# Performance work log

Measured on AMD Instinct MI355X. Metric: run time of the kernel, lower is better.

Reference implementation:

```python
import jax, jax.numpy as jnp
import numpy as np

B, S, D, H = 2, 2048, 2048, 16
Dh = D // H


def _rotate_interleaved(t):
    # t: (..., Dh); pairs (x0,x1) -> (-x1, x0), interleaved
    t2 = t.reshape(t.shape[:-1] + (Dh // 2, 2))
    rot = jnp.stack([-t2[..., 1], t2[..., 0]], axis=-1)
    return rot.reshape(t.shape)


def _apply_rope(t, cos, sin):
    # t: (B,H,S,Dh); cos/sin: (S,Dh) broadcast over batch and heads
    return t * cos[None, None, :, :] + _rotate_interleaved(t) * sin[None, None, :, :]


def setup_inputs() -> dict:
    key = jax.random.key(0)
    ks = jax.random.split(key, 4)
    x = jax.random.normal(ks[0], (B, S, D), dtype=jnp.float32)
    wq = jax.random.normal(ks[1], (D, D), dtype=jnp.float32) * (D ** -0.5)
    wk = jax.random.normal(ks[2], (D, D), dtype=jnp.float32) * (D ** -0.5)
    wv = jax.random.normal(ks[3], (D, D), dtype=jnp.float32) * (D ** -0.5)
    # Real RoPE cos/sin tables: theta_i = 10000^{-2i/Dh}, interleaved layout
    inv_freq = 1.0 / (10000.0 ** (np.arange(0, Dh, 2, dtype=np.float32) / Dh))
    angles = np.arange(S, dtype=np.float32)[:, None] * inv_freq[None, :]  # (S, Dh/2)
    angles = np.repeat(angles, 2, axis=-1)  # (S, Dh) interleaved
    rope_cos = jnp.asarray(np.cos(angles))
    rope_sin = jnp.asarray(np.sin(angles))
    return {"x": x, "wq": wq, "wk": wk, "wv": wv,
            "rope_cos": rope_cos, "rope_sin": rope_sin}


def reference(x, wq, wk, wv, rope_cos, rope_sin):
    b, s, d = x.shape
    # QKV projections (torch Linear: y = x @ W^T), split into heads -> (B,H,S,Dh)
    def proj(w):
        return (x @ w.T).reshape(b, s, H, Dh).transpose(0, 2, 1, 3)
    q, k, v = proj(wq), proj(wk), proj(wv)
    cos, sin = rope_cos[:s], rope_sin[:s]
    q = _apply_rope(q, cos, sin)
    k = _apply_rope(k, cos, sin)
    # causal SDPA
    scores = jnp.einsum('bhqd,bhkd->bhqk', q, k) / jnp.sqrt(jnp.float32(Dh))
    causal = jnp.tril(jnp.ones((s, s), dtype=bool))
    scores = jnp.where(causal[None, None], scores, jnp.float32(-1e30))
    attn = jax.nn.softmax(scores, axis=-1)
    out = jnp.einsum('bhqk,bhkd->bhqd', attn, v)  # (B,H,S,Dh)
    # extra trailing softmax over head dim (as in source)
    out = jax.nn.softmax(out.astype(jnp.float32), axis=-1)
    return out.transpose(0, 2, 1, 3).reshape(b, s, -1)
```

## Files before the change

### kernel.cpp

```cpp
#include <hip/hip_runtime.h>

#define Bc 2
#define Sc 2048
#define Dc 2048
#define Hc 16
#define DHc 128

typedef _Float16 f16;
typedef __attribute__((ext_vector_type(4))) _Float16 v4h;
typedef __attribute__((ext_vector_type(8))) _Float16 v8h;
typedef __attribute__((ext_vector_type(4))) float v4f;
typedef __attribute__((ext_vector_type(16))) float v16f;
typedef __attribute__((ext_vector_type(4))) float f32x4;

__global__ void cvt_kernel(const float* __restrict__ x, const float* __restrict__ wq,
                           const float* __restrict__ wk, const float* __restrict__ wv,
                           f16* __restrict__ xh, f16* __restrict__ wqh,
                           f16* __restrict__ wkh, f16* __restrict__ wvh)
{
    int bid = blockIdx.x;
    const float* src; f16* dst; int idx;
    if (bid < 8192)       { src = x;  dst = xh;  idx = bid; }
    else if (bid < 12288) { src = wq; dst = wqh; idx = bid - 8192; }
    else if (bid < 16384) { src = wk; dst = wkh; idx = bid - 12288; }
    else                  { src = wv; dst = wvh; idx = bid - 16384; }
    int i = idx * 256 + threadIdx.x;
    f32x4 v = ((const f32x4*)src)[i];
    v4h hv; hv[0]=(f16)v[0]; hv[1]=(f16)v[1]; hv[2]=(f16)v[2]; hv[3]=(f16)v[3];
    ((v4h*)dst)[i] = hv;
}

__launch_bounds__(256)
__global__ void proj_f16_kernel(const f16* __restrict__ xh, const f16* __restrict__ wqh,
                                const f16* __restrict__ wkh, const f16* __restrict__ wvh,
                                const float* __restrict__ cs, const float* __restrict__ sn,
                                f16* __restrict__ qh, f16* __restrict__ kh,
                                f16* __restrict__ vt)
{
    const int z = blockIdx.z;
    const f16* wh = (z == 0) ? wqh : ((z == 1) ? wkh : wvh);
    const int m0 = blockIdx.x * 128, n0 = blockIdx.y * 128;
    const int tid = threadIdx.x, lane = tid & 63, wid = tid >> 6;
    const int wm = wid >> 1, wn = wid & 1;
    const int l15 = lane & 15, quad = lane >> 4;
    const int lrow = lane >> 3, lcol = lane & 7;

    __shared__ __align__(16) f16 smem[128 * 136];
    f16 (*As)[64] = (f16(*)[64])smem;
    f16 (*Bs)[64] = (f16(*)[64])(smem + 8192);

    v4f acc[4][4];
    #pragma unroll
    for (int i = 0; i < 4; ++i)
        #pragma unroll
        for (int j = 0; j < 4; ++j)
            acc[i][j] = (v4f){0.f, 0.f, 0.f, 0.f};

    for (int k0 = 0; k0 < Dc; k0 += 64) {
        __syncthreads();
        #pragma unroll
        for (int i = 0; i < 4; ++i) {
            int g = wid * 4 + i;
            const f16* ga = xh + (size_t)(m0 + g * 8 + lrow) * Dc + k0 + lcol * 8;
            __builtin_amdgcn_global_load_lds(
                (const __attribute__((address_space(1))) void*)ga,
                (__attribute__((address_space(3))) void*)(smem + g * 512), 16, 0, 0);
            const f16* gb = wh + (size_t)(n0 + g * 8 + lrow) * Dc + k0 + lcol * 8;
            __builtin_amdgcn_global_load_lds(
                (const __attribute__((address_space(1))) void*)gb,
                (__attribute__((address_space(3))) void*)(smem + 8192 + g * 512), 16, 0, 0);
        }
        __syncthreads();
        #pragma unroll
        for (int kk = 0; kk < 2; ++kk) {
            v8h af[4], bf[4];
            #pragma unroll
            for (int mi = 0; mi < 4; ++mi)
                af[mi] = *(const v8h*)&As[wm * 64 + mi * 16 + l15][kk * 32 + quad * 8];
            #pragma unroll
            for (int ni = 0; ni < 4; ++ni)
                bf[ni] = *(const v8h*)&Bs[wn * 64 + ni * 16 + l15][kk * 32 + quad * 8];
            #pragma unroll
            for (int mi = 0; mi < 4; ++mi)
                #pragma unroll
                for (int ni = 0; ni < 4; ++ni)
                    acc[mi][ni] = __builtin_amdgcn_mfma_f32_16x16x32_f16(
                        af[mi], bf[ni], acc[mi][ni], 0, 0, 0);
        }
    }
    __syncthreads();

    f16 (*Ep)[136] = (f16(*)[136])smem;
    #pragma unroll
    for (int mi = 0; mi < 4; ++mi)
        #pragma unroll
        for (int ni = 0; ni < 4; ++ni)
            #pragma unroll
            for (int r = 0; r < 4; ++r) {
                int ml = wm * 64 + mi * 16 + quad * 4 + r;
                int nl = wn * 64 + ni * 16 + l15;
                f16 val = (f16)acc[mi][ni][r];
                if (z == 2) Ep[nl][ml] = val;
                else        Ep[ml][nl] = val;
            }
    __syncthreads();

    const int b = m0 >> 11, s0 = m0 & 2047, h = n0 >> 7;
    if (z < 2) {
        f16* outp = (z == 0) ? qh : kh;
        const float scl = (z == 0) ? 0.08838834764831845f : 1.0f;
        #pragma unroll
        for (int it = 0; it < 8; ++it) {
            int ch = tid + it * 256, row = ch >> 4, c = ch & 15;
            v8h val = *(const v8h*)&Ep[row][c * 8];
            int s = s0 + row;
            const float* cp = cs + (size_t)s * DHc + c * 8;
            const float* sp = sn + (size_t)s * DHc + c * 8;
            f32x4 ca = *(const f32x4*)cp, cb = *(const f32x4*)(cp + 4);
            f32x4 sa = *(const f32x4*)sp, sb = *(const f32x4*)(sp + 4);
            float v[8];
            #pragma unroll
            for (int j = 0; j < 8; ++j) v[j] = (float)val[j];
            v8h rv;
            rv[0] = (f16)((v[0]*ca[0] - v[1]*sa[0]) * scl);
            rv[1] = (f16)((v[1]*ca[1] + v[0]*sa[1]) * scl);
            rv[2] = (f16)((v[2]*ca[2] - v[3]*sa[2]) * scl);
            rv[3] = (f16)((v[3]*ca[3] + v[2]*sa[3]) * scl);
            rv[4] = (f16)((v[4]*cb[0] - v[5]*sb[0]) * scl);
            rv[5] = (f16)((v[5]*cb[1] + v[4]*sb[1]) * scl);
            rv[6] = (f16)((v[6]*cb[2] - v[7]*sb[2]) * scl);
            rv[7] = (f16)((v[7]*cb[3] + v[6]*sb[3]) * scl);
            *(v8h*)(outp + ((size_t)((b * Hc + h) * Sc) + s0 + row) * DHc + c * 8) = rv;
        }
    } else {
        #pragma unroll
        for (int it = 0; it < 8; ++it) {
            int ch = tid + it * 256, row = ch >> 4, c = ch & 15;
            *(v8h*)(vt + ((size_t)((b * Hc + h) * DHc) + row) * Sc + s0 + c * 8) =
                *(const v8h*)&Ep[row][c * 8];
        }
    }
}

__launch_bounds__(256)
__global__ void proj_kernel(const float* __restrict__ x, const float* __restrict__ wq,
                            const float* __restrict__ wk, const float* __restrict__ wv,
                            f16* __restrict__ qh, f16* __restrict__ kh, f16* __restrict__ vt)
{
    const int z = blockIdx.z;
    const float* w = (z == 0) ? wq : ((z == 1) ? wk : wv);
    const int m0 = blockIdx.x * 128, n0 = blockIdx.y * 128;
    const int tid = threadIdx.x, lane = tid & 63, wid = tid >> 6;
    const int wm = wid >> 1, wn = wid & 1;
    const int l15 = lane & 15, quad = lane >> 4;

    __shared__ __align__(16) f16 smem[2 * 128 * 72];
    f16 (*As)[72] = (f16(*)[72])smem;
    f16 (*Bs)[72] = (f16(*)[72])(smem + 128 * 72);

    v4f acc[4][4];
    for (int i = 0; i < 4; ++i)
        for (int j = 0; j < 4; ++j)
            acc[i][j] = (v4f){0.f, 0.f, 0.f, 0.f};

    for (int k0 = 0; k0 < Dc; k0 += 64) {
        __syncthreads();
        for (int it = 0; it < 4; ++it) {
            int chunk = tid + it * 256;
            int r = chunk >> 3, cc = chunk & 7;
            const f32x4* pa = (const f32x4*)(x + (size_t)(m0 + r) * Dc + k0 + cc * 8);
            f32x4 a0 = pa[0], a1 = pa[1];
            v8h ha;
            ha[0]=(f16)a0[0]; ha[1]=(f16)a0[1]; ha[2]=(f16)a0[2]; ha[3]=(f16)a0[3];
            ha[4]=(f16)a1[0]; ha[5]=(f16)a1[1]; ha[6]=(f16)a1[2]; ha[7]=(f16)a1[3];
            *(v8h*)&As[r][cc * 8] = ha;
            const f32x4* pb = (const f32x4*)(w + (size_t)(n0 + r) * Dc + k0 + cc * 8);
            f32x4 b0 = pb[0], b1 = pb[1];
            v8h hb;
            hb[0]=(f16)b0[0]; hb[1]=(f16)b0[1]; hb[2]=(f16)b0[2]; hb[3]=(f16)b0[3];
            hb[4]=(f16)b1[0]; hb[5]=(f16)b1[1]; hb[6]=(f16)b1[2]; hb[7]=(f16)b1[3];
            *(v8h*)&Bs[r][cc * 8] = hb;
        }
        __syncthreads();
        for (int kk = 0; kk < 2; ++kk) {
            v8h af[4], bf[4];
            for (int mi = 0; mi < 4; ++mi)
                af[mi] = *(const v8h*)&As[wm * 64 + mi * 16 + l15][kk * 32 + quad * 8];
            for (int ni = 0; ni < 4; ++ni)
                bf[ni] = *(const v8h*)&Bs[wn * 64 + ni * 16 + l15][kk * 32 + quad * 8];
            for (int mi = 0; mi < 4; ++mi)
                for (int ni = 0; ni < 4; ++ni)
                    acc[mi][ni] = __builtin_amdgcn_mfma_f32_16x16x32_f16(
                        af[mi], bf[ni], acc[mi][ni], 0, 0, 0);
        }
    }
    __syncthreads();
    f16 (*Ep)[136] = (f16(*)[136])smem;
    for (int mi = 0; mi < 4; ++mi)
        for (int ni = 0; ni < 4; ++ni)
            for (int r = 0; r < 4; ++r) {
                int ml = wm * 64 + mi * 16 + quad * 4 + r;
                int nl = wn * 64 + ni * 16 + l15;
                f16 val = (f16)acc[mi][ni][r];
                if (z == 2) Ep[nl][ml] = val;
                else        Ep[ml][nl] = val;
            }
    __syncthreads();
    const int b = m0 >> 11, s0 = m0 & 2047, h = n0 >> 7;
    if (z < 2) {
        f16* outp = (z == 0) ? qh : kh;
        for (int it = 0; it < 8; ++it) {
            int ch = tid + it * 256, row = ch >> 4, c = ch & 15;
            *(v8h*)(outp + ((size_t)((b * Hc + h) * Sc) + s0 + row) * DHc + c * 8) =
                *(const v8h*)&Ep[row][c * 8];
        }
    } else {
        for (int it = 0; it < 8; ++it) {
            int ch = tid + it * 256, row = ch >> 4, c = ch & 15;
            *(v8h*)(vt + ((size_t)((b * Hc + h) * DHc) + row) * Sc + s0 + c * 8) =
                *(const v8h*)&Ep[row][c * 8];
        }
    }
}

__global__ void rope_kernel(f16* __restrict__ qh, f16* __restrict__ kh,
                            const float* __restrict__ cs, const float* __restrict__ sn)
{
    int i  = blockIdx.x * 256 + threadIdx.x;
    int d2 = i & 63;
    int s  = (i >> 6) & (Sc - 1);
    int bh = i >> 17;
    f16* t = blockIdx.y ? kh : qh;
    float scale = blockIdx.y ? 1.0f : 0.08838834764831845f;
    float c  = cs[s * DHc + 2 * d2];
    float sv = sn[s * DHc + 2 * d2];
    f16* p = t + ((size_t)bh * Sc + s) * DHc + 2 * d2;
    float t0 = (float)p[0], t1 = (float)p[1];
    p[0] = (f16)((t0 * c - t1 * sv) * scale);
    p[1] = (f16)((t1 * c + t0 * sv) * scale);
}

__launch_bounds__(256, 2)
__global__ void attn_kernel(const f16* __restrict__ qh, const f16* __restrict__ kh,
                            const f16* __restrict__ vt, float* __restrict__ out)
{
    const int qt = 15 - blockIdx.x;
    const int bh = blockIdx.y;
    const int b = bh >> 4, h = bh & 15;
    const int tid = threadIdx.x, lane = tid & 63, w = tid >> 6;
    const int l31 = lane & 31, half = lane >> 5;

    __shared__ __align__(16) f16 smem[33792];
    f16* ksm = smem;
    f16* vsm = smem + 16384;

    const int q0 = qt * 128 + w * 32;
    const int qg = q0 + l31;
    const size_t bhoff = (size_t)bh * Sc * DHc;

    v8h qf[8];
    const f16* qrow = qh + bhoff + (size_t)qg * DHc;
    #pragma unroll
    for (int s = 0; s < 8; ++s)
        qf[s] = *(const v8h*)(qrow + s * 16 + half * 8);

    const f16* ksrc[4]; const f16* vsrc[4];
    f16* kdst[4]; f16* vdst[4];
    #pragma unroll
    for (int j = 0; j < 4; ++j) {
        int slot0 = j * 256 + w * 64;
        {   int r = (slot0 >> 4) + (lane >> 4);
            int c = (lane & 15) ^ (r & 7);
            ksrc[j] = kh + bhoff + (size_t)r * DHc + c * 8;
            kdst[j] = ksm + slot0 * 8; }
        {   int r = (slot0 >> 3) + (lane >> 3);
            int c = (lane & 7) ^ (r & 7);
            vsrc[j] = vt + bhoff + (size_t)r * Sc + c * 8;
            vdst[j] = vsm + slot0 * 8; }
    }

#define STAGE(kt_, buf_) do {                                                   \
        int _ko = (kt_) * 64 * DHc;                                             \
        int _vo = (kt_) * 64;                                                   \
        int _lb = (buf_) * 8192;                                                \
        _Pragma("unroll")                                                       \
        for (int j = 0; j < 4; ++j) {                                           \
            __builtin_amdgcn_global_load_lds(                                   \
                (const __attribute__((address_space(1))) void*)(ksrc[j] + _ko), \
                (__attribute__((address_space(3))) void*)(kdst[j] + _lb), 16, 0, 0); \
            __builtin_amdgcn_global_load_lds(                                   \
                (const __attribute__((address_space(1))) void*)(vsrc[j] + _vo), \
                (__attribute__((address_space(3))) void*)(vdst[j] + _lb), 16, 0, 0); \
        } } while (0)

    float l_run = 0.f;
    v16f o[4];
    #pragma unroll
    for (int i = 0; i < 4; ++i)
        #pragma unroll
        for (int r = 0; r < 16; ++r) o[i][r] = 0.f;

    const int sw = l31 & 7;
    const int nkt = 2 * qt + 2;

    STAGE(0, 0);
    for (int kt = 0; kt < nkt; ++kt) {
        __syncthreads();
        const int buf = kt & 1;
        if (kt + 1 < nkt) STAGE(kt + 1, buf ^ 1);
        if (q0 + 31 < kt * 64) continue;

        const f16* kbuf = ksm + buf * 8192;
        const f16* vbuf = vsm + buf * 8192;
        const bool do1 = (kt * 64 + 32 <= q0 + 31);

        v16f st0, st1;
        #pragma unroll
        for (int r = 0; r < 16; ++r) { st0[r] = 0.f; st1[r] = 0.f; }
        #pragma unroll
        for (int s = 0; s < 8; ++s) {
            int c = ((s * 2 + half) ^ sw) * 8;
            v8h kf0 = *(const v8h*)(kbuf + l31 * 128 + c);
            st0 = __builtin_amdgcn_mfma_f32_32x32x16_f16(kf0, qf[s], st0, 0, 0, 0);
            if (do1) {
                v8h kf1 = *(const v8h*)(kbuf + (32 + l31) * 128 + c);
                st1 = __builtin_amdgcn_mfma_f32_32x32x16_f16(kf1, qf[s], st1, 0, 0, 0);
            }
        }

        float sum = 0.f;
        #pragma unroll
        for (int r = 0; r < 16; ++r) {
            int key = kt * 64 + (r & 3) + 8 * (r >> 2) + 4 * half;
            float sv = (key > qg) ? -1e30f : st0[r];
            float p = __expf(sv);
            st0[r] = p; sum += p;
        }
        if (do1) {
            #pragma unroll
            for (int r = 0; r < 16; ++r) {
                int key = kt * 64 + 32 + (r & 3) + 8 * (r >> 2) + 4 * half;
                float sv = (key > qg) ? -1e30f : st1[r];
                float p = __expf(sv);
                st1[r] = p; sum += p;
            }
        }
        sum += __shfl_xor(sum, 32);
        l_run += sum;

        #pragma unroll
        for (int s2 = 0; s2 < 4; ++s2) {
            v4h bfr;
            bfr[0]=(f16)st0[4*s2]; bfr[1]=(f16)st0[4*s2+1];
            bfr[2]=(f16)st0[4*s2+2]; bfr[3]=(f16)st0[4*s2+3];
            int c = ((s2 ^ sw) * 8) + half * 4;
            #pragma unroll
            for (int dt = 0; dt < 4; ++dt) {
                v4h vf = *(const v4h*)(vbuf + (dt * 32 + l31) * 64 + c);
                o[dt] = __builtin_amdgcn_mfma_f32_32x32x8f16(vf, bfr, o[dt], 0, 0, 0);
            }
        }
        if (do1) {
            #pragma unroll
            for (int s2 = 0; s2 < 4; ++s2) {
                v4h bfr;
                bfr[0]=(f16)st1[4*s2]; bfr[1]=(f16)st1[4*s2+1];
                bfr[2]=(f16)st1[4*s2+2]; bfr[3]=(f16)st1[4*s2+3];
                int c = (((4 + s2) ^ sw) * 8) + half * 4;
                #pragma unroll
                for (int dt = 0; dt < 4; ++dt) {
                    v4h vf = *(const v4h*)(vbuf + (dt * 32 + l31) * 64 + c);
                    o[dt] = __builtin_amdgcn_mfma_f32_32x32x8f16(vf, bfr, o[dt], 0, 0, 0);
                }
            }
        }
    }
#undef STAGE

    float inv = 1.f / l_run;
    float mxd = -1e30f;
    #pragma unroll
    for (int dt = 0; dt < 4; ++dt)
        #pragma unroll
        for (int r = 0; r < 16; ++r) {
            o[dt][r] *= inv;
            mxd = fmaxf(mxd, o[dt][r]);
        }
    mxd = fmaxf(mxd, __shfl_xor(mxd, 32));
    float sd = 0.f;
    #pragma unroll
    for (int dt = 0; dt < 4; ++dt)
        #pragma unroll
        for (int r = 0; r < 16; ++r) {
            float t = __expf(o[dt][r] - mxd);
            o[dt][r] = t;
            sd += t;
        }
    sd += __shfl_xor(sd, 32);
    float rinv = 1.f / sd;

    __syncthreads();
    float* os = (float*)smem + w * (32 * 132);
    #pragma unroll
    for (int dt = 0; dt < 4; ++dt)
        #pragma unroll
        for (int r = 0; r < 16; ++r) {
            int dh = dt * 32 + (r & 3) + 8 * (r >> 2) + 4 * half;
            os[l31 * 132 + dh] = o[dt][r] * rinv;
        }
    __syncthreads();
    #pragma unroll
    for (int step = 0; step < 16; ++step) {
        int row = step * 2 + half;
        f32x4 vv = *(const f32x4*)(os - (size_t)half * 0 + row * 132 + l31 * 4);
        *(f32x4*)(out + ((size_t)(b * Sc + q0 + row)) * Dc + h * DHc + l31 * 4) = vv;
    }
}

extern "C" void kernel_launch(void* const* d_in, const int* in_sizes, int n_in,
                              void* d_out, int out_size, void* d_ws, size_t ws_size,
                              hipStream_t stream)
{
    const float* x  = (const float*)d_in[0];
    const float* wq = (const float*)d_in[1];
    const float* wk = (const float*)d_in[2];
    const float* wv = (const float*)d_in[3];
    const float* cs = (const float*)d_in[4];
    const float* sn = (const float*)d_in[5];
    float* out = (float*)d_out;

    const size_t tsz = (size_t)Bc * Hc * Sc * DHc;
    f16* qh = (f16*)d_ws;
    f16* kh = qh + tsz;
    f16* vt = kh + tsz;

    if (ws_size >= 11 * tsz) {
        f16* xh  = vt + tsz;
        f16* wqh = xh + tsz;
        f16* wkh = wqh + tsz / 2;
        f16* wvh = wkh + tsz / 2;
        cvt_kernel<<<20480, 256, 0, stream>>>(x, wq, wk, wv, xh, wqh, wkh, wvh);
        proj_f16_kernel<<<dim3(32, 16, 3), 256, 0, stream>>>(xh, wqh, wkh, wvh,
                                                             cs, sn, qh, kh, vt);
    } else {
        proj_kernel<<<dim3(32, 16, 3), 256, 0, stream>>>(x, wq, wk, wv, qh, kh, vt);
        rope_kernel<<<dim3(16384, 2), 256, 0, stream>>>(qh, kh, cs, sn);
    }
    attn_kernel<<<dim3(16, 32), 256, 0, stream>>>(qh, kh, vt, out);
}
```

Measured before the change: 364.7 us.

## Load K directly from global, shrink LDS to V only, raise occupancy

K fragments are now read straight from global memory per wave instead of being staged through LDS, so shared memory holds only the double-buffered V tiles (32KB instead of ~66KB). The launch bound goes from 2 to 3 blocks per SM. The output epilogue writes float4s from registers to global directly, dropping the LDS transpose and its two barriers. The trade-off is more global/L2 traffic for K, with K loads sitting on the MFMA critical path without prefetch, tighter register limits at 3 blocks, and less coalesced output stores.

```diff
diff --git a/kernel.cpp b/kernel.cpp
--- a/kernel.cpp
+++ b/kernel.cpp
@@ -240,7 +240,7 @@
     p[1] = (f16)((t1 * c + t0 * sv) * scale);
 }
 
-__launch_bounds__(256, 2)
+__launch_bounds__(256, 3)
 __global__ void attn_kernel(const f16* __restrict__ qh, const f16* __restrict__ kh,
                             const f16* __restrict__ vt, float* __restrict__ out)
 {
@@ -250,9 +250,7 @@
     const int tid = threadIdx.x, lane = tid & 63, w = tid >> 6;
     const int l31 = lane & 31, half = lane >> 5;
 
-    __shared__ __align__(16) f16 smem[33792];
-    f16* ksm = smem;
-    f16* vsm = smem + 16384;
+    __shared__ __align__(16) f16 vsm[2 * 8192];
 
     const int q0 = qt * 128 + w * 32;
     const int qg = q0 + l31;
@@ -264,33 +262,22 @@
     for (int s = 0; s < 8; ++s)
         qf[s] = *(const v8h*)(qrow + s * 16 + half * 8);
 
-    const f16* ksrc[4]; const f16* vsrc[4];
-    f16* kdst[4]; f16* vdst[4];
-    #pragma unroll
-    for (int j = 0; j < 4; ++j) {
-        int slot0 = j * 256 + w * 64;
-        {   int r = (slot0 >> 4) + (lane >> 4);
-            int c = (lane & 15) ^ (r & 7);
-            ksrc[j] = kh + bhoff + (size_t)r * DHc + c * 8;
-            kdst[j] = ksm + slot0 * 8; }
-        {   int r = (slot0 >> 3) + (lane >> 3);
-            int c = (lane & 7) ^ (r & 7);
-            vsrc[j] = vt + bhoff + (size_t)r * Sc + c * 8;
-            vdst[j] = vsm + slot0 * 8; }
-    }
-
-#define STAGE(kt_, buf_) do {                                                   \
-        int _ko = (kt_) * 64 * DHc;                                             \
-        int _vo = (kt_) * 64;                                                   \
-        int _lb = (buf_) * 8192;                                                \
-        _Pragma("unroll")                                                       \
-        for (int j = 0; j < 4; ++j) {                                           \
-            __builtin_amdgcn_global_load_lds(                                   \
-                (const __attribute__((address_space(1))) void*)(ksrc[j] + _ko), \
-                (__attribute__((address_space(3))) void*)(kdst[j] + _lb), 16, 0, 0); \
-            __builtin_amdgcn_global_load_lds(                                   \
-                (const __attribute__((address_space(1))) void*)(vsrc[j] + _vo), \
-                (__attribute__((address_space(3))) void*)(vdst[j] + _lb), 16, 0, 0); \
+    const f16* kb0 = kh + bhoff + (size_t)l31 * DHc + half * 8;
+    const f16* kb1 = kb0 + 32 * DHc;
+
+    const int vr = w * 8 + (lane >> 3);
+    const int vc = (lane & 7) ^ ((lane >> 3) & 7);
+    const f16* vsrc0 = vt + bhoff + (size_t)vr * Sc + vc * 8;
+    const int vdst0 = (w * 64) * 8;
+
+#define STAGEV(kt_, buf_) do {                                                     \
+        _Pragma("unroll")                                                          \
+        for (int j = 0; j < 4; ++j) {                                              \
+            __builtin_amdgcn_global_load_lds(                                      \
+                (const __attribute__((address_space(1))) void*)                    \
+                    (vsrc0 + (size_t)(j * 32) * Sc + (kt_) * 64),                  \
+                (__attribute__((address_space(3))) void*)                          \
+                    (vsm + (buf_) * 8192 + vdst0 + j * 2048), 16, 0, 0);           \
         } } while (0)
 
     float l_run = 0.f;
@@ -303,27 +290,27 @@
     const int sw = l31 & 7;
     const int nkt = 2 * qt + 2;
 
-    STAGE(0, 0);
+    STAGEV(0, 0);
     for (int kt = 0; kt < nkt; ++kt) {
         __syncthreads();
         const int buf = kt & 1;
-        if (kt + 1 < nkt) STAGE(kt + 1, buf ^ 1);
+        if (kt + 1 < nkt) STAGEV(kt + 1, buf ^ 1);
         if (q0 + 31 < kt * 64) continue;
 
-        const f16* kbuf = ksm + buf * 8192;
         const f16* vbuf = vsm + buf * 8192;
         const bool do1 = (kt * 64 + 32 <= q0 + 31);
+        const f16* k0p = kb0 + (size_t)kt * 64 * DHc;
+        const f16* k1p = kb1 + (size_t)kt * 64 * DHc;
 
         v16f st0, st1;
         #pragma unroll
         for (int r = 0; r < 16; ++r) { st0[r] = 0.f; st1[r] = 0.f; }
         #pragma unroll
         for (int s = 0; s < 8; ++s) {
-            int c = ((s * 2 + half) ^ sw) * 8;
-            v8h kf0 = *(const v8h*)(kbuf + l31 * 128 + c);
+            v8h kf0 = *(const v8h*)(k0p + s * 16);
             st0 = __builtin_amdgcn_mfma_f32_32x32x16_f16(kf0, qf[s], st0, 0, 0, 0);
             if (do1) {
-                v8h kf1 = *(const v8h*)(kbuf + (32 + l31) * 128 + c);
+                v8h kf1 = *(const v8h*)(k1p + s * 16);
                 st1 = __builtin_amdgcn_mfma_f32_32x32x16_f16(kf1, qf[s], st1, 0, 0, 0);
             }
         }
@@ -375,7 +362,7 @@
             }
         }
     }
-#undef STAGE
+#undef STAGEV
 
     float inv = 1.f / l_run;
     float mxd = -1e30f;
@@ -399,22 +386,18 @@
     sd += __shfl_xor(sd, 32);
     float rinv = 1.f / sd;
 
-    __syncthreads();
-    float* os = (float*)smem + w * (32 * 132);
+    float* orow = out + (size_t)(b * Sc + qg) * Dc + h * DHc;
     #pragma unroll
     for (int dt = 0; dt < 4; ++dt)
         #pragma unroll
-        for (int r = 0; r < 16; ++r) {
-            int dh = dt * 32 + (r & 3) + 8 * (r >> 2) + 4 * half;
-            os[l31 * 132 + dh] = o[dt][r] * rinv;
-        }
-    __syncthreads();
-    #pragma unroll
-    for (int step = 0; step < 16; ++step) {
-        int row = step * 2 + half;
-        f32x4 vv = *(const f32x4*)(os - (size_t)half * 0 + row * 132 + l31 * 4);
-        *(f32x4*)(out + ((size_t)(b * Sc + q0 + row)) * Dc + h * DHc + l31 * 4) = vv;
-    }
+        for (int g = 0; g < 4; ++g) {
+            f32x4 vv;
+            vv[0] = o[dt][4*g+0] * rinv;
+            vv[1] = o[dt][4*g+1] * rinv;
+            vv[2] = o[dt][4*g+2] * rinv;
+            vv[3] = o[dt][4*g+3] * rinv;
+            *(f32x4*)(orow + dt * 32 + g * 8 + half * 4) = vv;
+        }
 }
 
 extern "C" void kernel_launch(void* const* d_in, const int* in_sizes, int n_in,
```

New measurement: 463.0 us. 1.27x slower.

## Pair complementary causal query tiles per block for balanced attention work

Applied to the files above, without the earlier changes.

Each attention block now processes two query tiles (qt and 15-qt), so every block does the same amount of causal work, and only 256 blocks are launched instead of 512. K/V staging continues seamlessly across the two phases. The output epilogue writes directly from registers rather than going through a shared-memory transpose, which removes two barriers and the extra LDS use. In exchange each block runs serially longer, and the direct stores are less coalesced.

```diff
diff --git a/kernel.cpp b/kernel.cpp
--- a/kernel.cpp
+++ b/kernel.cpp
@@ -244,25 +244,20 @@
 __global__ void attn_kernel(const f16* __restrict__ qh, const f16* __restrict__ kh,
                             const f16* __restrict__ vt, float* __restrict__ out)
 {
-    const int qt = 15 - blockIdx.x;
-    const int bh = blockIdx.y;
+    const int L = blockIdx.x;
+    const int slot = L >> 3;
+    const int bh = (L & 7) * 4 + (slot >> 3);
+    const int p  = slot & 7;
     const int b = bh >> 4, h = bh & 15;
     const int tid = threadIdx.x, lane = tid & 63, w = tid >> 6;
     const int l31 = lane & 31, half = lane >> 5;
-
-    __shared__ __align__(16) f16 smem[33792];
+    const int sw = l31 & 7;
+
+    __shared__ __align__(16) f16 smem[32768];
     f16* ksm = smem;
     f16* vsm = smem + 16384;
 
-    const int q0 = qt * 128 + w * 32;
-    const int qg = q0 + l31;
     const size_t bhoff = (size_t)bh * Sc * DHc;
-
-    v8h qf[8];
-    const f16* qrow = qh + bhoff + (size_t)qg * DHc;
-    #pragma unroll
-    for (int s = 0; s < 8; ++s)
-        qf[s] = *(const v8h*)(qrow + s * 16 + half * 8);
 
     const f16* ksrc[4]; const f16* vsrc[4];
     f16* kdst[4]; f16* vdst[4];
@@ -293,128 +288,145 @@
                 (__attribute__((address_space(3))) void*)(vdst[j] + _lb), 16, 0, 0); \
         } } while (0)
 
-    float l_run = 0.f;
-    v16f o[4];
-    #pragma unroll
-    for (int i = 0; i < 4; ++i)
-        #pragma unroll
-        for (int r = 0; r < 16; ++r) o[i][r] = 0.f;
-
-    const int sw = l31 & 7;
-    const int nkt = 2 * qt + 2;
-
+    const int qtA = 15 - p;
+    const int nktA = 2 * qtA + 2;
+
+    int ibuf = 0;
     STAGE(0, 0);
-    for (int kt = 0; kt < nkt; ++kt) {
-        __syncthreads();
-        const int buf = kt & 1;
-        if (kt + 1 < nkt) STAGE(kt + 1, buf ^ 1);
-        if (q0 + 31 < kt * 64) continue;
-
-        const f16* kbuf = ksm + buf * 8192;
-        const f16* vbuf = vsm + buf * 8192;
-        const bool do1 = (kt * 64 + 32 <= q0 + 31);
-
-        v16f st0, st1;
-        #pragma unroll
-        for (int r = 0; r < 16; ++r) { st0[r] = 0.f; st1[r] = 0.f; }
-        #pragma unroll
-        for (int s = 0; s < 8; ++s) {
-            int c = ((s * 2 + half) ^ sw) * 8;
-            v8h kf0 = *(const v8h*)(kbuf + l31 * 128 + c);
-            st0 = __builtin_amdgcn_mfma_f32_32x32x16_f16(kf0, qf[s], st0, 0, 0, 0);
+
+    #pragma unroll 1
+    for (int ph = 0; ph < 2; ++ph) {
+        const int qt  = ph ? p : qtA;
+        const int nkt = 2 * qt + 2;
+        const int q0  = qt * 128 + w * 32;
+        const int qg  = q0 + l31;
+
+        v8h qf[8];
+        const f16* qrow = qh + bhoff + (size_t)qg * DHc;
+        #pragma unroll
+        for (int s = 0; s < 8; ++s)
+            qf[s] = *(const v8h*)(qrow + s * 16 + half * 8);
+
+        float l_run = 0.f;
+        v16f o[4];
+        #pragma unroll
+        for (int i = 0; i < 4; ++i)
+            #pragma unroll
+            for (int r = 0; r < 16; ++r) o[i][r] = 0.f;
+
+        #pragma unroll 1
+        for (int kt = 0; kt < nkt; ++kt, ++ibuf) {
+            __syncthreads();
+            const int buf = ibuf & 1;
+            const int ni = ibuf + 1;
+            if (ni < 34) {
+                int tn = (ni < nktA) ? ni : ni - nktA;
+                STAGE(tn, ni & 1);
+            }
+            if (q0 + 31 < kt * 64) continue;
+
+            const f16* kbuf = ksm + buf * 8192;
+            const f16* vbuf = vsm + buf * 8192;
+            const bool do1 = (kt * 64 + 32 <= q0 + 31);
+
+            v16f st0, st1;
+            #pragma unroll
+            for (int r = 0; r < 16; ++r) { st0[r] = 0.f; st1[r] = 0.f; }
+            #pragma unroll
+            for (int s = 0; s < 8; ++s) {
+                int c = ((s * 2 + half) ^ sw) * 8;
+                v8h kf0 = *(const v8h*)(kbuf + l31 * 128 + c);
+                st0 = __builtin_amdgcn_mfma_f32_32x32x16_f16(kf0, qf[s], st0, 0, 0, 0);
+                if (do1) {
+                    v8h kf1 = *(const v8h*)(kbuf + (32 + l31) * 128 + c);
+                    st1 = __builtin_amdgcn_mfma_f32_32x32x16_f16(kf1, qf[s], st1, 0, 0, 0);
+                }
+            }
+
+            float sum = 0.f;
+            #pragma unroll
+            for (int r = 0; r < 16; ++r) {
+                int key = kt * 64 + (r & 3) + 8 * (r >> 2) + 4 * half;
+                float sv = (key > qg) ? -1e30f : st0[r];
+                float pe = __expf(sv);
+                st0[r] = pe; sum += pe;
+            }
             if (do1) {
-                v8h kf1 = *(const v8h*)(kbuf + (32 + l31) * 128 + c);
-                st1 = __builtin_amdgcn_mfma_f32_32x32x16_f16(kf1, qf[s], st1, 0, 0, 0);
-            }
-        }
-
-        float sum = 0.f;
-        #pragma unroll
-        for (int r = 0; r < 16; ++r) {
-            int key = kt * 64 + (r & 3) + 8 * (r >> 2) + 4 * half;
-            float sv = (key > qg) ? -1e30f : st0[r];
-            float p = __expf(sv);
-            st0[r] = p; sum += p;
-        }
-        if (do1) {
-            #pragma unroll
-            for (int r = 0; r < 16; ++r) {
-                int key = kt * 64 + 32 + (r & 3) + 8 * (r >> 2) + 4 * half;
-                float sv = (key > qg) ? -1e30f : st1[r];
-                float p = __expf(sv);
-                st1[r] = p; sum += p;
-            }
-        }
-        sum += __shfl_xor(sum, 32);
-        l_run += sum;
-
-        #pragma unroll
-        for (int s2 = 0; s2 < 4; ++s2) {
-            v4h bfr;
-            bfr[0]=(f16)st0[4*s2]; bfr[1]=(f16)st0[4*s2+1];
-            bfr[2]=(f16)st0[4*s2+2]; bfr[3]=(f16)st0[4*s2+3];
-            int c = ((s2 ^ sw) * 8) + half * 4;
-            #pragma unroll
-            for (int dt = 0; dt < 4; ++dt) {
-                v4h vf = *(const v4h*)(vbuf + (dt * 32 + l31) * 64 + c);
-                o[dt] = __builtin_amdgcn_mfma_f32_32x32x8f16(vf, bfr, o[dt], 0, 0, 0);
-            }
-        }
-        if (do1) {
+                #pragma unroll
+                for (int r = 0; r < 16; ++r) {
+                    int key = kt * 64 + 32 + (r & 3) + 8 * (r >> 2) + 4 * half;
+                    float sv = (key > qg) ? -1e30f : st1[r];
+                    float pe = __expf(sv);
+                    st1[r] = pe; sum += pe;
+                }
+            }
+            sum += __shfl_xor(sum, 32);
+            l_run += sum;
+
             #pragma unroll
             for (int s2 = 0; s2 < 4; ++s2) {
                 v4h bfr;
-                bfr[0]=(f16)st1[4*s2]; bfr[1]=(f16)st1[4*s2+1];
-                bfr[2]=(f16)st1[4*s2+2]; bfr[3]=(f16)st1[4*s2+3];
-                int c = (((4 + s2) ^ sw) * 8) + half * 4;
+                bfr[0]=(f16)st0[4*s2]; bfr[1]=(f16)st0[4*s2+1];
+                bfr[2]=(f16)st0[4*s2+2]; bfr[3]=(f16)st0[4*s2+3];
+                int c = ((s2 ^ sw) * 8) + half * 4;
                 #pragma unroll
                 for (int dt = 0; dt < 4; ++dt) {
                     v4h vf = *(const v4h*)(vbuf + (dt * 32 + l31) * 64 + c);
                     o[dt] = __builtin_amdgcn_mfma_f32_32x32x8f16(vf, bfr, o[dt], 0, 0, 0);
                 }
             }
-        }
+            if (do1) {
+                #pragma unroll
+                for (int s2 = 0; s2 < 4; ++s2) {
+                    v4h bfr;
+                    bfr[0]=(f16)st1[4*s2]; bfr[1]=(f16)st1[4*s2+1];
+                    bfr[2]=(f16)st1[4*s2+2]; bfr[3]=(f16)st1[4*s2+3];
+                    int c = (((4 + s2) ^ sw) * 8) + half * 4;
+                    #pragma unroll
+                    for (int dt = 0; dt < 4; ++dt) {
+                        v4h vf = *(const v4h*)(vbuf + (dt * 32 + l31) * 64 + c);
+                        o[dt] = __builtin_amdgcn_mfma_f32_32x32x8f16(vf, bfr, o[dt], 0, 0, 0);
+                    }
+                }
+            }
+        }
+
+        float inv = 1.f / l_run;
+        float mxd = -1e30f;
+        #pragma unroll
+        for (int dt = 0; dt < 4; ++dt)
+            #pragma unroll
+            for (int r = 0; r < 16; ++r) {
+                o[dt][r] *= inv;
+                mxd = fmaxf(mxd, o[dt][r]);
+            }
+        mxd = fmaxf(mxd, __shfl_xor(mxd, 32));
+        float sd = 0.f;
+        #pragma unroll
+        for (int dt = 0; dt < 4; ++dt)
+            #pragma unroll
+            for (int r = 0; r < 16; ++r) {
+                float t = __expf(o[dt][r] - mxd);
+                o[dt][r] = t;
+                sd += t;
+            }
+        sd += __shfl_xor(sd, 32);
+        float rinv = 1.f / sd;
+
+        float* orow = out + (size_t)(b * Sc + qg) * Dc + h * DHc;
+        #pragma unroll
+        for (int dt = 0; dt < 4; ++dt)
+            #pragma unroll
+            for (int g = 0; g < 4; ++g) {
+                f32x4 vv;
+                vv[0] = o[dt][4*g+0] * rinv;
+                vv[1] = o[dt][4*g+1] * rinv;
+                vv[2] = o[dt][4*g+2] * rinv;
+                vv[3] = o[dt][4*g+3] * rinv;
+                *(f32x4*)(orow + dt * 32 + g * 8 + half * 4) = vv;
+            }
     }
 #undef STAGE
-
-    float inv = 1.f / l_run;
-    float mxd = -1e30f;
-    #pragma unroll
-    for (int dt = 0; dt < 4; ++dt)
-        #pragma unroll
-        for (int r = 0; r < 16; ++r) {
-            o[dt][r] *= inv;
-            mxd = fmaxf(mxd, o[dt][r]);
-        }
-    mxd = fmaxf(mxd, __shfl_xor(mxd, 32));
-    float sd = 0.f;
-    #pragma unroll
-    for (int dt = 0; dt < 4; ++dt)
-        #pragma unroll
-        for (int r = 0; r < 16; ++r) {
-            float t = __expf(o[dt][r] - mxd);
-            o[dt][r] = t;
-            sd += t;
-        }
-    sd += __shfl_xor(sd, 32);
-    float rinv = 1.f / sd;
-
-    __syncthreads();
-    float* os = (float*)smem + w * (32 * 132);
-    #pragma unroll
-    for (int dt = 0; dt < 4; ++dt)
-        #pragma unroll
-        for (int r = 0; r < 16; ++r) {
-            int dh = dt * 32 + (r & 3) + 8 * (r >> 2) + 4 * half;
-            os[l31 * 132 + dh] = o[dt][r] * rinv;
-        }
-    __syncthreads();
-    #pragma unroll
-    for (int step = 0; step < 16; ++step) {
-        int row = step * 2 + half;
-        f32x4 vv = *(const f32x4*)(os - (size_t)half * 0 + row * 132 + l31 * 4);
-        *(f32x4*)(out + ((size_t)(b * Sc + q0 + row)) * Dc + h * DHc + l31 * 4) = vv;
-    }
 }
 
 extern "C" void kernel_launch(void* const* d_in, const int* in_sizes, int n_in,
@@ -446,5 +458,5 @@
         proj_kernel<<<dim3(32, 16, 3), 256, 0, stream>>>(x, wq, wk, wv, qh, kh, vt);
         rope_kernel<<<dim3(16384, 2), 256, 0, stream>>>(qh, kh, cs, sn);
     }
-    attn_kernel<<<dim3(16, 32), 256, 0, stream>>>(qh, kh, vt, out);
-}
+    attn_kernel<<<256, 256, 0, stream>>>(qh, kh, vt, out);
+}
```

Measured after the change: 356.3 us. -2.3%, faster.
